# Kernel tuning notes

Measured on AMD Instinct MI355X. Metric: run time of the kernel, lower is better.

## Reference

```python
import jax, jax.numpy as jnp
import numpy as np

L, H = 6, 8          # n_layer, n_head
LN_EPS = 1e-5


def _ln(x, g, b):
    mu = jnp.mean(x, axis=-1, keepdims=True)
    var = jnp.mean((x - mu) ** 2, axis=-1, keepdims=True)
    return (x - mu) * jax.lax.rsqrt(var + LN_EPS) * g + b


def setup_inputs() -> dict:
    key = jax.random.key(0)
    B, T, V, D = 2, 2048, 32000, 512
    F = 4 * D
    std = 0.02
    ks = jax.random.split(key, 8)
    idx = jax.random.randint(ks[0], (B, T), 0, V)
    wte = jax.random.normal(ks[1], (V, D), dtype=jnp.float32) * std
    wpe = jax.random.normal(ks[2], (T, D), dtype=jnp.float32) * std
    qkv_w = jax.random.normal(ks[3], (L, D, 3 * D), dtype=jnp.float32) * std
    proj_w = jax.random.normal(ks[4], (L, D, D), dtype=jnp.float32) * std
    fc1_w = jax.random.normal(ks[5], (L, D, F), dtype=jnp.float32) * std
    fc2_w = jax.random.normal(ks[6], (L, F, D), dtype=jnp.float32) * std
    return dict(
        idx=idx, wte=wte, wpe=wpe,
        ln1_g=jnp.ones((L, D), jnp.float32), ln1_b=jnp.zeros((L, D), jnp.float32),
        qkv_w=qkv_w, qkv_b=jnp.zeros((L, 3 * D), jnp.float32),
        proj_w=proj_w, proj_b=jnp.zeros((L, D), jnp.float32),
        ln2_g=jnp.ones((L, D), jnp.float32), ln2_b=jnp.zeros((L, D), jnp.float32),
        fc1_w=fc1_w, fc1_b=jnp.zeros((L, F), jnp.float32),
        fc2_w=fc2_w, fc2_b=jnp.zeros((L, D), jnp.float32),
        lnf_g=jnp.ones((D,), jnp.float32), lnf_b=jnp.zeros((D,), jnp.float32),
    )


def reference(idx, wte, wpe, ln1_g, ln1_b, qkv_w, qkv_b, proj_w, proj_b,
              ln2_g, ln2_b, fc1_w, fc1_b, fc2_w, fc2_b, lnf_g, lnf_b):
    B, T = idx.shape
    D = wte.shape[1]
    hd = D // H
    scale = 1.0 / jnp.sqrt(jnp.asarray(hd, wte.dtype))
    x = wte[idx] + wpe[:T]                      # [B,T,D]
    mask = jnp.tril(jnp.ones((T, T), dtype=bool))

    def block(x, p):
        g1, b1, Wqkv, bqkv, Wp, bp, g2, b2, W1, bf1, W2, bf2 = p
        h = _ln(x, g1, b1)
        qkv = h @ Wqkv + bqkv                   # [B,T,3D]
        q, k, v = jnp.split(qkv, 3, axis=-1)
        q = q.reshape(B, T, H, hd)
        k = k.reshape(B, T, H, hd)
        v = v.reshape(B, T, H, hd)
        att = jnp.einsum('bqhd,bkhd->bhqk', q, k) * scale
        att = jnp.where(mask, att, -jnp.inf)
        att = jax.nn.softmax(att, axis=-1)
        y = jnp.einsum('bhqk,bkhd->bqhd', att, v).reshape(B, T, D)
        x = x + y @ Wp + bp
        h = _ln(x, g2, b2)
        x = x + jax.nn.gelu(h @ W1 + bf1, approximate=False) @ W2 + bf2
        return x, None

    x, _ = jax.lax.scan(block, x, (ln1_g, ln1_b, qkv_w, qkv_b, proj_w, proj_b,
                                   ln2_g, ln2_b, fc1_w, fc1_b, fc2_w, fc2_b))
    x = _ln(x, lnf_g, lnf_b)
    logits = x @ wte.T                          # tied head, [B,T,V]
    return logits
```

## Files before the change

### kernel.cpp

```cpp
#include <hip/hip_runtime.h>
#include <hip/hip_bf16.h>
#include <math.h>

#define BB 2
#define TT 2048
#define DD 512
#define HH 8
#define HD 64
#define FF 2048
#define VV 32000
#define LL 6
#define MM (BB * TT)

typedef unsigned int   u32;
typedef unsigned short u16;
typedef __attribute__((ext_vector_type(8))) short short8;
typedef __attribute__((ext_vector_type(4))) float f32x4;

__device__ __forceinline__ u16 f2bf_bits(float f)
{
    __hip_bfloat16 h = __float2bfloat16(f);
    u16 u;
    __builtin_memcpy(&u, &h, 2);
    return u;
}

__device__ __forceinline__ void gll16(const u16* g, u16* l)
{
    __builtin_amdgcn_global_load_lds(
        (const __attribute__((address_space(1))) u32*)g,
        (__attribute__((address_space(3))) u32*)l,
        16, 0, 0);
}

__device__ __forceinline__ float gelu_exact(float v)
{
    return 0.5f * v * (1.0f + erff(v * 0.70710678118654752440f));
}

__device__ __forceinline__ u16* swp(u16* base, int row, int col)
{
    int off = (row * 128 + col * 2) ^ ((row & 7) << 4);
    return (u16*)((char*)base + off);
}
__device__ __forceinline__ const u16* swpc(const u16* base, int row, int col)
{
    int off = (row * 128 + col * 2) ^ ((row & 7) << 4);
    return (const u16*)((const char*)base + off);
}

template<int CTRL>
__device__ __forceinline__ float fmax_dpp(float v)
{
    union { float f; int i; } a, b;
    a.f = v;
    b.i = __builtin_amdgcn_mov_dpp(a.i, CTRL, 0xf, 0xf, true);
    return fmaxf(v, b.f);
}

__global__ __launch_bounds__(128)
void embed_kernel(const int* __restrict__ idx, const float* __restrict__ wte,
                  const float* __restrict__ wpe, float* __restrict__ x)
{
    int row = blockIdx.x;
    int t = row & (TT - 1);
    int tok = idx[row];
    const float4* wt = (const float4*)(wte + (size_t)tok * DD);
    const float4* wp = (const float4*)(wpe + (size_t)t * DD);
    float4 a = wt[threadIdx.x];
    float4 p = wp[threadIdx.x];
    float4 r;
    r.x = a.x + p.x; r.y = a.y + p.y; r.z = a.z + p.z; r.w = a.w + p.w;
    ((float4*)(x + (size_t)row * DD))[threadIdx.x] = r;
}

__global__ __launch_bounds__(256)
void ln_kernel(const float* __restrict__ x, const float* __restrict__ g,
               const float* __restrict__ b, u16* __restrict__ out)
{
    int row = blockIdx.x;
    const float* xr = x + (size_t)row * DD;
    int tid = threadIdx.x;
    float v1 = xr[tid], v2 = xr[tid + 256];
    float s = v1 + v2;
    float ss = v1 * v1 + v2 * v2;
    #pragma unroll
    for (int o = 32; o; o >>= 1) {
        s  += __shfl_xor(s, o);
        ss += __shfl_xor(ss, o);
    }
    __shared__ float sred[4], ssred[4];
    int wid = tid >> 6, lane = tid & 63;
    if (lane == 0) { sred[wid] = s; ssred[wid] = ss; }
    __syncthreads();
    s  = sred[0] + sred[1] + sred[2] + sred[3];
    ss = ssred[0] + ssred[1] + ssred[2] + ssred[3];
    float mu  = s * (1.0f / DD);
    float var = ss * (1.0f / DD) - mu * mu;
    float rs  = rsqrtf(var + 1e-5f);
    u16* orow = out + (size_t)row * DD;
    orow[tid]       = f2bf_bits((v1 - mu) * rs * g[tid]       + b[tid]);
    orow[tid + 256] = f2bf_bits((v2 - mu) * rs * g[tid + 256] + b[tid + 256]);
}

__global__ __launch_bounds__(256)
void weight_prep_kernel(const float* __restrict__ qkv_w, const float* __restrict__ proj_w,
                        const float* __restrict__ fc1_w, const float* __restrict__ fc2_w,
                        u16* __restrict__ wqa, u16* __restrict__ wpa,
                        u16* __restrict__ w1a, u16* __restrict__ w2a)
{
    int id = blockIdx.x;
    int l = id / 3072, r = id % 3072;
    const float* in; u16* out; int K, N, tt;
    if (r < 768)       { in = qkv_w + (size_t)l * DD * 3 * DD; out = wqa + (size_t)l * 3 * DD * DD; K = DD; N = 3 * DD; tt = r; }
    else if (r < 1024) { in = proj_w + (size_t)l * DD * DD;    out = wpa + (size_t)l * DD * DD;    K = DD; N = DD;     tt = r - 768; }
    else if (r < 2048) { in = fc1_w + (size_t)l * DD * FF;     out = w1a + (size_t)l * DD * FF;    K = DD; N = FF;     tt = r - 1024; }
    else               { in = fc2_w + (size_t)l * FF * DD;     out = w2a + (size_t)l * FF * DD;    K = FF; N = DD;     tt = r - 2048; }
    int ntx = N >> 5;
    int n0 = (tt % ntx) << 5, k0 = (tt / ntx) << 5;
    __shared__ float tile[32][33];
    int tx = threadIdx.x & 31, ty = threadIdx.x >> 5;
    #pragma unroll
    for (int i = 0; i < 4; ++i)
        tile[ty + i * 8][tx] = in[(size_t)(k0 + ty + i * 8) * N + n0 + tx];
    __syncthreads();
    #pragma unroll
    for (int i = 0; i < 4; ++i)
        out[(size_t)(n0 + ty + i * 8) * K + k0 + tx] = f2bf_bits(tile[tx][ty + i * 8]);
}

__global__ __launch_bounds__(256)
void cvt_kernel(const float* __restrict__ in, u16* __restrict__ out, int n4)
{
    int i = blockIdx.x * 256 + threadIdx.x;
    if (i >= n4) return;
    float4 v = ((const float4*)in)[i];
    ushort4 o;
    o.x = f2bf_bits(v.x); o.y = f2bf_bits(v.y);
    o.z = f2bf_bits(v.z); o.w = f2bf_bits(v.w);
    ((ushort4*)out)[i] = o;
}

template<int BN, bool GELU_ACT, bool RESID, bool OUTBF16, bool QKV_SPLIT>
__global__ __launch_bounds__(256)
void mfma_gemm(const u16* __restrict__ A, const u16* __restrict__ Bt,
               const float* __restrict__ bias, const float* __restrict__ resid,
               void* __restrict__ Cout, u16* __restrict__ Vout,
               int M, int N, int K)
{
    constexpr int NJ = BN / 32;
    __shared__ u16 As[2][128 * 64];
    __shared__ u16 Bs[2][BN * 64];

    const int tid  = threadIdx.x;
    const int lane = tid & 63;
    const int w    = tid >> 6;
    const int wr   = w >> 1, wc = w & 1;

    const int nbx = gridDim.x;
    const int nwg = nbx * gridDim.y;
    int bid = blockIdx.y * nbx + blockIdx.x;
    int swz = (bid & 7) * (nwg >> 3) + (bid >> 3);
    const int m0 = (swz / nbx) * 128;
    const int n0 = (swz % nbx) * BN;

    const int trow = tid >> 3;
    const int tcol = (tid & 7) * 8;
    const u16* ga = A  + (size_t)(m0 + trow) * K + tcol;
    const u16* gb = Bt + (size_t)(n0 + trow) * K + tcol;

    auto stage = [&](int buf, int k0) {
        u16* la = As[buf] + tid * 8;
        u16* lb = Bs[buf] + tid * 8;
        #pragma unroll
        for (int p = 0; p < 4; ++p)
            gll16(ga + k0 + (size_t)p * 32 * K, la + p * 2048);
        #pragma unroll
        for (int p = 0; p < NJ; ++p)
            gll16(gb + k0 + (size_t)p * 32 * K, lb + p * 2048);
    };

    f32x4 acc[4][NJ] = {};

    const int fr = lane & 15;
    const int fk = (lane >> 4) * 8;

    const int nt = K >> 6;
    stage(0, 0);
    for (int t = 0; t < nt; ++t) {
        asm volatile("s_waitcnt vmcnt(0)" ::: "memory");
        __syncthreads();
        if (t + 1 < nt) stage((t + 1) & 1, (t + 1) << 6);

        const u16* as = As[t & 1];
        const u16* bs = Bs[t & 1];
        #pragma unroll
        for (int ks = 0; ks < 2; ++ks) {
            short8 af[4], bfr[NJ];
            #pragma unroll
            for (int f = 0; f < 4; ++f)
                af[f]  = *(const short8*)&as[(wr * 64 + f * 16 + fr) * 64 + ks * 32 + fk];
            #pragma unroll
            for (int f = 0; f < NJ; ++f)
                bfr[f] = *(const short8*)&bs[(wc * (BN / 2) + f * 16 + fr) * 64 + ks * 32 + fk];
            #pragma unroll
            for (int i = 0; i < 4; ++i)
                #pragma unroll
                for (int j = 0; j < NJ; ++j)
                    acc[i][j] = __builtin_amdgcn_mfma_f32_16x16x32_bf16(
                        af[i], bfr[j], acc[i][j], 0, 0, 0);
        }
    }

    const int c0 = n0 + wc * (BN / 2) + fr;
    const int r0 = m0 + wr * 64 + ((lane >> 4) << 2);
    #pragma unroll
    for (int j = 0; j < NJ; ++j) {
        const int c = c0 + j * 16;
        const float bv = bias ? bias[c] : 0.0f;
        #pragma unroll
        for (int i = 0; i < 4; ++i) {
            const int row0 = r0 + i * 16;
            if constexpr (QKV_SPLIT) {
                if (c < 1024) {
                    #pragma unroll
                    for (int r = 0; r < 4; ++r)
                        ((u16*)Cout)[(size_t)(row0 + r) * 1024 + c] =
                            f2bf_bits(acc[i][j][r] + bv);
                } else {
                    const int t0 = row0 & (TT - 1);
                    const size_t vrow = ((size_t)(row0 >> 11) * 512 + (c - 1024)) << 11;
                    const int pb = (t0 & ~63) | (((t0 & 15) << 2) | ((t0 >> 4) & 3));
                    Vout[vrow + pb]      = f2bf_bits(acc[i][j][0] + bv);
                    Vout[vrow + pb + 4]  = f2bf_bits(acc[i][j][1] + bv);
                    Vout[vrow + pb + 8]  = f2bf_bits(acc[i][j][2] + bv);
                    Vout[vrow + pb + 12] = f2bf_bits(acc[i][j][3] + bv);
                }
            } else {
                #pragma unroll
                for (int r = 0; r < 4; ++r) {
                    const int row = row0 + r;
                    float v = acc[i][j][r] + bv;
                    if constexpr (GELU_ACT) v = gelu_exact(v);
                    if constexpr (RESID) v += resid[(size_t)row * N + c];
                    if constexpr (OUTBF16)
                        ((u16*)Cout)[(size_t)row * N + c] = f2bf_bits(v);
                    else
                        ((float*)Cout)[(size_t)row * N + c] = v;
                }
            }
        }
    }
}

__global__ __launch_bounds__(256)
void attn_kernel(const u16* __restrict__ qkb, const u16* __restrict__ vtb,
                 u16* __restrict__ y)
{
    const int l = blockIdx.x;
    const int u = l & 255, v = l >> 8;
    const int bh = u & 15;
    const int half = u >> 4;
    const int qt = v ? (16 + half) : (15 - half);
    const int h = bh & (HH - 1);
    const int b = bh >> 3;

    __shared__ alignas(16) u16 Qs[4096];
    __shared__ alignas(16) u16 Ks[2][4096];
    __shared__ alignas(16) u16 Vt[2][4096];
    __shared__ alignas(16) u16 Ps[4096];

    const int tid = threadIdx.x;
    const int lane = tid & 63;
    const int w = tid >> 6;
    const int ln = lane & 15, hi = lane >> 4;
    const int q0 = qt * 64;

    const u16* base  = qkb + (size_t)b * TT * 1024 + h * HD;
    const u16* vbase = vtb + (size_t)(b * 512 + h * HD) * TT;

    const int sr = tid >> 2, sc = (tid & 3) * 16;

    {
        const u16* qrow = base + (size_t)(q0 + sr) * 1024;
        *(short8*)swp(Qs, sr, sc)     = *(const short8*)(qrow + sc);
        *(short8*)swp(Qs, sr, sc + 8) = *(const short8*)(qrow + sc + 8);
    }
    short8 rk0, rk1, rv0, rv1;
    {
        const u16* krow = base + (size_t)sr * 1024 + 512;
        rk0 = *(const short8*)(krow + sc);
        rk1 = *(const short8*)(krow + sc + 8);
        const u16* vrow = vbase + (size_t)sr * TT;
        rv0 = *(const short8*)(vrow + sc);
        rv1 = *(const short8*)(vrow + sc + 8);
    }
    __syncthreads();

    short8 aq0 = *(const short8*)swpc(Qs, w * 16 + ln, hi * 8);
    short8 aq1 = *(const short8*)swpc(Qs, w * 16 + ln, 32 + hi * 8);

    const float SC = 0.18033688011112042f;

    float m[4], lsum[4];
    f32x4 oacc[4] = {};
    #pragma unroll
    for (int r = 0; r < 4; ++r) { m[r] = -INFINITY; lsum[r] = 0.0f; }

    for (int kt = 0; kt <= qt; ++kt) {
        u16* ks = Ks[kt & 1];
        u16* vt = Vt[kt & 1];

        *(short8*)swp(ks, sr, sc)     = rk0;
        *(short8*)swp(ks, sr, sc + 8) = rk1;
        *(short8*)swp(vt, sr, sc)     = rv0;
        *(short8*)swp(vt, sr, sc + 8) = rv1;
        __syncthreads();

        if (kt < qt) {
            const int k0n = (kt + 1) * 64;
            const u16* krow = base + (size_t)(k0n + sr) * 1024 + 512;
            rk0 = *(const short8*)(krow + sc);
            rk1 = *(const short8*)(krow + sc + 8);
            const u16* vrow = vbase + (size_t)sr * TT + k0n;
            rv0 = *(const short8*)(vrow + sc);
            rv1 = *(const short8*)(vrow + sc + 8);
        }

        f32x4 sacc[4] = {};
        __builtin_amdgcn_s_setprio(1);
        #pragma unroll
        for (int j = 0; j < 4; ++j) {
            short8 bk0 = *(const short8*)swpc(ks, j * 16 + ln, hi * 8);
            short8 bk1 = *(const short8*)swpc(ks, j * 16 + ln, 32 + hi * 8);
            sacc[j] = __builtin_amdgcn_mfma_f32_16x16x32_bf16(aq0, bk0, sacc[j], 0, 0, 0);
            sacc[j] = __builtin_amdgcn_mfma_f32_16x16x32_bf16(aq1, bk1, sacc[j], 0, 0, 0);
        }
        __builtin_amdgcn_s_setprio(0);

        const bool diag = (kt == qt);
        #pragma unroll
        for (int r = 0; r < 4; ++r) {
            const int qrow = w * 16 + hi * 4 + r;
            float sv[4];
            #pragma unroll
            for (int j = 0; j < 4; ++j) sv[j] = sacc[j][r] * SC;
            if (diag) {
                #pragma unroll
                for (int j = 0; j < 4; ++j)
                    if (j * 16 + ln > qrow) sv[j] = -INFINITY;
            }
            float rm = fmaxf(fmaxf(sv[0], sv[1]), fmaxf(sv[2], sv[3]));
            rm = fmax_dpp<0x121>(rm);
            rm = fmax_dpp<0x122>(rm);
            rm = fmax_dpp<0x124>(rm);
            rm = fmax_dpp<0x128>(rm);
            if (rm > m[r]) {
                float corr = exp2f(m[r] - rm);
                m[r] = rm;
                lsum[r] *= corr;
                #pragma unroll
                for (int db = 0; db < 4; ++db) oacc[db][r] *= corr;
            }
            const float mn = m[r];
            float p0 = exp2f(sv[0] - mn);
            float p1 = exp2f(sv[1] - mn);
            float p2 = exp2f(sv[2] - mn);
            float p3 = exp2f(sv[3] - mn);
            u32 pk0 = (u32)f2bf_bits(p0) | ((u32)f2bf_bits(p1) << 16);
            u32 pk1 = (u32)f2bf_bits(p2) | ((u32)f2bf_bits(p3) << 16);
            char* pdst = (char*)Ps + (((qrow << 7) + (ln << 3)) ^ ((qrow & 7) << 4));
            uint2 pv; pv.x = pk0; pv.y = pk1;
            *(uint2*)pdst = pv;
            lsum[r] += (p0 + p1) + (p2 + p3);
        }

        short8 ap0 = *(const short8*)swpc(Ps, w * 16 + ln, hi * 8);
        short8 ap1 = *(const short8*)swpc(Ps, w * 16 + ln, 32 + hi * 8);
        __builtin_amdgcn_s_setprio(1);
        #pragma unroll
        for (int db = 0; db < 4; ++db) {
            short8 bv0 = *(const short8*)swpc(vt, db * 16 + ln, hi * 8);
            short8 bv1 = *(const short8*)swpc(vt, db * 16 + ln, 32 + hi * 8);
            oacc[db] = __builtin_amdgcn_mfma_f32_16x16x32_bf16(ap0, bv0, oacc[db], 0, 0, 0);
            oacc[db] = __builtin_amdgcn_mfma_f32_16x16x32_bf16(ap1, bv1, oacc[db], 0, 0, 0);
        }
        __builtin_amdgcn_s_setprio(0);
    }

    #pragma unroll
    for (int r = 0; r < 4; ++r) {
        float lt = lsum[r];
        #pragma unroll
        for (int o = 1; o < 16; o <<= 1) lt += __shfl_xor(lt, o);
        const int q = q0 + w * 16 + hi * 4 + r;
        const float inv = 1.0f / lt;
        u16* yrow = y + (size_t)(b * TT + q) * DD + h * HD;
        #pragma unroll
        for (int db = 0; db < 4; ++db)
            yrow[db * 16 + ln] = f2bf_bits(oacc[db][r] * inv);
    }
}

extern "C" void kernel_launch(void* const* d_in, const int* in_sizes, int n_in,
                              void* d_out, int out_size, void* d_ws, size_t ws_size,
                              hipStream_t stream)
{
    const int*   idx    = (const int*)  d_in[0];
    const float* wte    = (const float*)d_in[1];
    const float* wpe    = (const float*)d_in[2];
    const float* ln1_g  = (const float*)d_in[3];
    const float* ln1_b  = (const float*)d_in[4];
    const float* qkv_w  = (const float*)d_in[5];
    const float* qkv_b  = (const float*)d_in[6];
    const float* proj_w = (const float*)d_in[7];
    const float* proj_b = (const float*)d_in[8];
    const float* ln2_g  = (const float*)d_in[9];
    const float* ln2_b  = (const float*)d_in[10];
    const float* fc1_w  = (const float*)d_in[11];
    const float* fc1_b  = (const float*)d_in[12];
    const float* fc2_w  = (const float*)d_in[13];
    const float* fc2_b  = (const float*)d_in[14];
    const float* lnf_g  = (const float*)d_in[15];
    const float* lnf_b  = (const float*)d_in[16];
    float* out = (float*)d_out;

    char* ws = (char*)d_ws;
    float* x    = (float*)(ws);
    u16*   h    = (u16*)(ws + ((size_t)8  << 20));
    u16*   y    = (u16*)(ws + ((size_t)12 << 20));
    u16*   qkb  = (u16*)(ws + ((size_t)16 << 20));
    u16*   vtb  = (u16*)(ws + ((size_t)24 << 20));
    u16*   wqa  = (u16*)(ws + ((size_t)28 << 20));
    u16*   wpa  = (u16*)(ws + ((size_t)38 << 20));
    u16*   w1a  = (u16*)(ws + ((size_t)42 << 20));
    u16*   w2a  = (u16*)(ws + ((size_t)55 << 20));
    u16*   ffb  = (u16*)(ws + ((size_t)68 << 20));
    u16*   wteb = (u16*)(ws + ((size_t)85 << 20));

    embed_kernel<<<MM, 128, 0, stream>>>(idx, wte, wpe, x);

    weight_prep_kernel<<<LL * 3072, 256, 0, stream>>>(
        qkv_w, proj_w, fc1_w, fc2_w, wqa, wpa, w1a, w2a);

    cvt_kernel<<<(VV * DD / 4 + 255) / 256, 256, 0, stream>>>(wte, wteb, VV * DD / 4);

    for (int l = 0; l < LL; ++l) {
        ln_kernel<<<MM, 256, 0, stream>>>(x, ln1_g + l * DD, ln1_b + l * DD, h);

        mfma_gemm<128, false, false, true, true><<<dim3(12, 32), 256, 0, stream>>>(
            h, wqa + (size_t)l * 3 * DD * DD, qkv_b + (size_t)l * 3 * DD,
            nullptr, qkb, vtb, MM, 3 * DD, DD);

        attn_kernel<<<512, 256, 0, stream>>>(qkb, vtb, y);

        mfma_gemm<64, false, true, false, false><<<dim3(8, 32), 256, 0, stream>>>(
            y, wpa + (size_t)l * DD * DD, proj_b + (size_t)l * DD,
            x, x, nullptr, MM, DD, DD);

        ln_kernel<<<MM, 256, 0, stream>>>(x, ln2_g + l * DD, ln2_b + l * DD, h);

        mfma_gemm<128, true, false, true, false><<<dim3(16, 32), 256, 0, stream>>>(
            h, w1a + (size_t)l * DD * FF, fc1_b + (size_t)l * FF,
            nullptr, ffb, nullptr, MM, FF, DD);

        mfma_gemm<64, false, true, false, false><<<dim3(8, 32), 256, 0, stream>>>(
            ffb, w2a + (size_t)l * FF * DD, fc2_b + (size_t)l * DD,
            x, x, nullptr, MM, DD, FF);
    }

    ln_kernel<<<MM, 256, 0, stream>>>(x, lnf_g, lnf_b, h);

    mfma_gemm<128, false, false, false, false><<<dim3(250, 32), 256, 0, stream>>>(
        h, wteb, nullptr, nullptr, out, nullptr, MM, VV, DD);
}
```

Measured before the change: 1.201 ms.

## Load attention K/V MFMA operands straight from global into registers, dropping LDS staging

The attention kernel stops staging Q, K and V tiles through shared memory with block-wide barriers. Each wave now loads its MFMA operand fragments for Q, K and V directly from global memory into registers, prefetching the next K tile while the softmax runs. The QKV GEMM epilogue changes the transposed V layout from a permuted order to plain token order and writes it with 4-wide vector stores. The P-tile LDS write becomes four scalar swizzled stores instead of one packed 8-byte store. This removes barriers and LDS traffic, but every wave now fetches the same K/V tile from global/L2 separately, with less coalesced accesses and more register pressure.

```diff
diff --git a/kernel.cpp b/kernel.cpp
--- a/kernel.cpp
+++ b/kernel.cpp
@@ -228,13 +228,13 @@
                         ((u16*)Cout)[(size_t)(row0 + r) * 1024 + c] =
                             f2bf_bits(acc[i][j][r] + bv);
                 } else {
+                    ushort4 o;
+                    o.x = f2bf_bits(acc[i][j][0] + bv);
+                    o.y = f2bf_bits(acc[i][j][1] + bv);
+                    o.z = f2bf_bits(acc[i][j][2] + bv);
+                    o.w = f2bf_bits(acc[i][j][3] + bv);
                     const int t0 = row0 & (TT - 1);
-                    const size_t vrow = ((size_t)(row0 >> 11) * 512 + (c - 1024)) << 11;
-                    const int pb = (t0 & ~63) | (((t0 & 15) << 2) | ((t0 >> 4) & 3));
-                    Vout[vrow + pb]      = f2bf_bits(acc[i][j][0] + bv);
-                    Vout[vrow + pb + 4]  = f2bf_bits(acc[i][j][1] + bv);
-                    Vout[vrow + pb + 8]  = f2bf_bits(acc[i][j][2] + bv);
-                    Vout[vrow + pb + 12] = f2bf_bits(acc[i][j][3] + bv);
+                    *(ushort4*)&Vout[(((size_t)(row0 >> 11) * 512 + (c - 1024)) << 11) + t0] = o;
                 }
             } else {
                 #pragma unroll
@@ -265,9 +265,6 @@
     const int h = bh & (HH - 1);
     const int b = bh >> 3;
 
-    __shared__ alignas(16) u16 Qs[4096];
-    __shared__ alignas(16) u16 Ks[2][4096];
-    __shared__ alignas(16) u16 Vt[2][4096];
     __shared__ alignas(16) u16 Ps[4096];
 
     const int tid = threadIdx.x;
@@ -279,26 +276,20 @@
     const u16* base  = qkb + (size_t)b * TT * 1024 + h * HD;
     const u16* vbase = vtb + (size_t)(b * 512 + h * HD) * TT;
 
-    const int sr = tid >> 2, sc = (tid & 3) * 16;
-
+    const u16* qrow = base + (size_t)(q0 + w * 16 + ln) * 1024;
+    short8 aq0 = *(const short8*)(qrow + hi * 8);
+    short8 aq1 = *(const short8*)(qrow + 32 + hi * 8);
+
+    short8 kb[8];
     {
-        const u16* qrow = base + (size_t)(q0 + sr) * 1024;
-        *(short8*)swp(Qs, sr, sc)     = *(const short8*)(qrow + sc);
-        *(short8*)swp(Qs, sr, sc + 8) = *(const short8*)(qrow + sc + 8);
-    }
-    short8 rk0, rk1, rv0, rv1;
-    {
-        const u16* krow = base + (size_t)sr * 1024 + 512;
-        rk0 = *(const short8*)(krow + sc);
-        rk1 = *(const short8*)(krow + sc + 8);
-        const u16* vrow = vbase + (size_t)sr * TT;
-        rv0 = *(const short8*)(vrow + sc);
-        rv1 = *(const short8*)(vrow + sc + 8);
-    }
-    __syncthreads();
-
-    short8 aq0 = *(const short8*)swpc(Qs, w * 16 + ln, hi * 8);
-    short8 aq1 = *(const short8*)swpc(Qs, w * 16 + ln, 32 + hi * 8);
+        const u16* kr = base + 512;
+        #pragma unroll
+        for (int j = 0; j < 4; ++j) {
+            const u16* p = kr + (size_t)(j * 16 + ln) * 1024 + hi * 8;
+            kb[j * 2]     = *(const short8*)(p);
+            kb[j * 2 + 1] = *(const short8*)(p + 32);
+        }
+    }
 
     const float SC = 0.18033688011112042f;
 
@@ -308,47 +299,47 @@
     for (int r = 0; r < 4; ++r) { m[r] = -INFINITY; lsum[r] = 0.0f; }
 
     for (int kt = 0; kt <= qt; ++kt) {
-        u16* ks = Ks[kt & 1];
-        u16* vt = Vt[kt & 1];
-
-        *(short8*)swp(ks, sr, sc)     = rk0;
-        *(short8*)swp(ks, sr, sc + 8) = rk1;
-        *(short8*)swp(vt, sr, sc)     = rv0;
-        *(short8*)swp(vt, sr, sc + 8) = rv1;
-        __syncthreads();
-
-        if (kt < qt) {
-            const int k0n = (kt + 1) * 64;
-            const u16* krow = base + (size_t)(k0n + sr) * 1024 + 512;
-            rk0 = *(const short8*)(krow + sc);
-            rk1 = *(const short8*)(krow + sc + 8);
-            const u16* vrow = vbase + (size_t)sr * TT + k0n;
-            rv0 = *(const short8*)(vrow + sc);
-            rv1 = *(const short8*)(vrow + sc + 8);
+        const int k0 = kt * 64;
+
+        short8 vb[8];
+        #pragma unroll
+        for (int db = 0; db < 4; ++db) {
+            const u16* p = vbase + (size_t)(db * 16 + ln) * TT + k0 + hi * 8;
+            vb[db * 2]     = *(const short8*)(p);
+            vb[db * 2 + 1] = *(const short8*)(p + 32);
         }
 
         f32x4 sacc[4] = {};
         __builtin_amdgcn_s_setprio(1);
         #pragma unroll
         for (int j = 0; j < 4; ++j) {
-            short8 bk0 = *(const short8*)swpc(ks, j * 16 + ln, hi * 8);
-            short8 bk1 = *(const short8*)swpc(ks, j * 16 + ln, 32 + hi * 8);
-            sacc[j] = __builtin_amdgcn_mfma_f32_16x16x32_bf16(aq0, bk0, sacc[j], 0, 0, 0);
-            sacc[j] = __builtin_amdgcn_mfma_f32_16x16x32_bf16(aq1, bk1, sacc[j], 0, 0, 0);
+            sacc[j] = __builtin_amdgcn_mfma_f32_16x16x32_bf16(aq0, kb[j * 2],     sacc[j], 0, 0, 0);
+            sacc[j] = __builtin_amdgcn_mfma_f32_16x16x32_bf16(aq1, kb[j * 2 + 1], sacc[j], 0, 0, 0);
         }
         __builtin_amdgcn_s_setprio(0);
 
+        short8 kn[8];
+        if (kt < qt) {
+            const u16* kr = base + (size_t)(k0 + 64) * 1024 + 512;
+            #pragma unroll
+            for (int j = 0; j < 4; ++j) {
+                const u16* p = kr + (size_t)(j * 16 + ln) * 1024 + hi * 8;
+                kn[j * 2]     = *(const short8*)(p);
+                kn[j * 2 + 1] = *(const short8*)(p + 32);
+            }
+        }
+
         const bool diag = (kt == qt);
         #pragma unroll
         for (int r = 0; r < 4; ++r) {
-            const int qrow = w * 16 + hi * 4 + r;
+            const int qr = w * 16 + hi * 4 + r;
             float sv[4];
             #pragma unroll
             for (int j = 0; j < 4; ++j) sv[j] = sacc[j][r] * SC;
             if (diag) {
                 #pragma unroll
                 for (int j = 0; j < 4; ++j)
-                    if (j * 16 + ln > qrow) sv[j] = -INFINITY;
+                    if (j * 16 + ln > qr) sv[j] = -INFINITY;
             }
             float rm = fmaxf(fmaxf(sv[0], sv[1]), fmaxf(sv[2], sv[3]));
             rm = fmax_dpp<0x121>(rm);
@@ -367,11 +358,10 @@
             float p1 = exp2f(sv[1] - mn);
             float p2 = exp2f(sv[2] - mn);
             float p3 = exp2f(sv[3] - mn);
-            u32 pk0 = (u32)f2bf_bits(p0) | ((u32)f2bf_bits(p1) << 16);
-            u32 pk1 = (u32)f2bf_bits(p2) | ((u32)f2bf_bits(p3) << 16);
-            char* pdst = (char*)Ps + (((qrow << 7) + (ln << 3)) ^ ((qrow & 7) << 4));
-            uint2 pv; pv.x = pk0; pv.y = pk1;
-            *(uint2*)pdst = pv;
+            *swp(Ps, qr, ln)      = f2bf_bits(p0);
+            *swp(Ps, qr, 16 + ln) = f2bf_bits(p1);
+            *swp(Ps, qr, 32 + ln) = f2bf_bits(p2);
+            *swp(Ps, qr, 48 + ln) = f2bf_bits(p3);
             lsum[r] += (p0 + p1) + (p2 + p3);
         }
 
@@ -380,12 +370,15 @@
         __builtin_amdgcn_s_setprio(1);
         #pragma unroll
         for (int db = 0; db < 4; ++db) {
-            short8 bv0 = *(const short8*)swpc(vt, db * 16 + ln, hi * 8);
-            short8 bv1 = *(const short8*)swpc(vt, db * 16 + ln, 32 + hi * 8);
-            oacc[db] = __builtin_amdgcn_mfma_f32_16x16x32_bf16(ap0, bv0, oacc[db], 0, 0, 0);
-            oacc[db] = __builtin_amdgcn_mfma_f32_16x16x32_bf16(ap1, bv1, oacc[db], 0, 0, 0);
+            oacc[db] = __builtin_amdgcn_mfma_f32_16x16x32_bf16(ap0, vb[db * 2],     oacc[db], 0, 0, 0);
+            oacc[db] = __builtin_amdgcn_mfma_f32_16x16x32_bf16(ap1, vb[db * 2 + 1], oacc[db], 0, 0, 0);
         }
         __builtin_amdgcn_s_setprio(0);
+
+        if (kt < qt) {
+            #pragma unroll
+            for (int i = 0; i < 8; ++i) kb[i] = kn[i];
+        }
     }
 
     #pragma unroll
```

Result: slower. 1.256 ms (+4.6%).
